# Kernel optimization log

Hardware: AMD Instinct MI355X
Metric: run time of the kernel (lower is better)

The kernel has to match this reference:

```python
import jax, jax.numpy as jnp
import numpy as np
from jax import lax

H, W = 4096, 4096

def setup_inputs() -> dict:
    key = jax.random.key(0)
    k_occ, k_seed = jax.random.split(key)
    occupied = (jax.random.uniform(k_occ, (H, W)) < 0.3).astype(jnp.float32)
    flood = ((jax.random.uniform(k_seed, (H, W)) < 1e-3).astype(jnp.float32)
             * (1.0 - occupied))
    flood_input = jnp.stack([occupied, flood], axis=-1)  # [H, W, 2]
    flood_count = jnp.zeros((H, W), dtype=jnp.float32)
    # Fixed flood kernel, HWIO layout: (3, 3, in=2, out=1)
    kernel = jnp.zeros((3, 3, 2, 1), dtype=jnp.float32)
    kernel = kernel.at[1, 1, 0, 0].set(-5.0)  # occupied center blocks flood
    kernel = kernel.at[1, 2, 1, 0].set(1.0)   # right
    kernel = kernel.at[2, 1, 1, 0].set(1.0)   # down
    kernel = kernel.at[1, 0, 1, 0].set(1.0)   # left
    kernel = kernel.at[0, 1, 1, 0].set(1.0)   # up
    kernel = kernel.at[1, 1, 1, 0].set(1.0)   # center
    bias = jnp.zeros((1,), dtype=jnp.float32)
    return {"flood_input": flood_input, "flood_count": flood_count,
            "kernel": kernel, "bias": bias, "num_steps": 16}

def reference(flood_input, flood_count, kernel, bias, num_steps):
    dn = ("NHWC", "HWIO", "NHWC")

    def flood_step(carry, _):
        x, count = carry                      # x: [H, W, 2], count: [H, W]
        occupied = x[..., 0]
        y = lax.conv_general_dilated(x[None], kernel, (1, 1), "SAME",
                                     dimension_numbers=dn)[0, ..., 0] + bias[0]
        y = jnp.clip(y, 0.0, 1.0)             # flooded frontier
        new_x = jnp.stack([occupied, y], axis=-1)
        return (new_x, count + y), None

    (x_final, count_final), _ = lax.scan(flood_step,
                                         (flood_input, flood_count),
                                         None, length=num_steps)
    # [H, W, 3]: occupied, flood, count
    return jnp.concatenate([x_final, count_final[..., None]], axis=-1)
```

## Files before the change

### kernel.cpp

```cpp
#include <hip/hip_runtime.h>


typedef unsigned long long u64;

#define HH 4096
#define WW 4096
#define WPR 64
#define NSTEPS 16
#define HALO 16
#define IT 32

__global__ __launch_bounds__(256) void pack_kernel(
    const float* __restrict__ flood_input,
    u64* __restrict__ occP, u64* __restrict__ flP)
{
    const int lane = threadIdx.x & 63;
    const int wv   = threadIdx.x >> 6;
    const int r    = blockIdx.x;
#pragma unroll
    for (int b = 0; b < 2; ++b) {
        float vx[8], vy[8];
#pragma unroll
        for (int j = 0; j < 8; ++j) {
            const int w = wv * 16 + b * 8 + j;
            const float2 v = *(const float2*)(flood_input +
                                ((size_t)r * WW + (w << 6) + lane) * 2);
            vx[j] = v.x; vy[j] = v.y;
        }
#pragma unroll
        for (int j = 0; j < 8; ++j) {
            const int w = wv * 16 + b * 8 + j;
            const u64 om = __ballot(vx[j] > 0.5f);
            const u64 fm = __ballot(vy[j] > 0.5f);
            if (lane == 0) {
                occP[(size_t)r * WPR + w] = om;
                flP [(size_t)r * WPR + w] = fm;
            }
        }
    }
}

__global__ __launch_bounds__(256, 8) void flood_kernel(
    const u64* __restrict__ occP, const u64* __restrict__ flP,
    const float* __restrict__ flood_count,
    float* __restrict__ out)
{
    __shared__ u64 plane[4][IT][7];
    __shared__ float out2[4][2 * 128 * 3];

    const int tid  = threadIdx.x;
    const int lane = tid & 63;
    const int wv   = tid >> 6;

    const int tile_r0 = blockIdx.y * IT;
    const int tile_c0 = blockIdx.x * (4 * IT) + wv * IT;
    const int bc0    = blockIdx.x * (4 * IT);

    const int gr  = tile_r0 - HALO + lane;
    const bool rin = (gr >= 0) & (gr < HH);
    const int s   = tile_c0 - HALO;
    const int q0  = ((s + 64) >> 6) - 1;
    const int sh  = s - (q0 << 6);

    const size_t base = (size_t)(rin ? gr : 0) * WPR;
    const int qa = min(max(q0, 0), WPR - 1);
    const int qb = min(max(q0 + 1, 0), WPR - 1);
    u64 o0 = occP[base + qa], o1 = occP[base + qb];
    u64 f0 = flP [base + qa], f1 = flP [base + qb];
    const bool va = rin & (q0 >= 0);
    const bool vb = rin & (q0 + 1 < WPR);
    if (!va) { o0 = ~0ull; f0 = 0ull; }
    if (!vb) { o1 = ~0ull; f1 = 0ull; }
    const u64 occ = (o0 >> sh) | (sh ? (o1 << (64 - sh)) : 0ull);
    u64       f   = (f0 >> sh) | (sh ? (f1 << (64 - sh)) : 0ull);

    const u64 nocc = ~occ;
    u64 c0 = 0, c1 = 0, c2 = 0, c3 = 0, c4 = 0;
#pragma unroll
    for (int it = 0; it < NSTEPS; ++it) {
        u64 up = __shfl_up(f, 1);
        u64 dn = __shfl_down(f, 1);
        if (lane == 0)  up = 0ull;
        if (lane == 63) dn = 0ull;
        f = nocc & (f | (f << 1) | (f >> 1) | up | dn);
        u64 c = f, t;
        t = c0; c0 = t ^ c; c = t & c;
        t = c1; c1 = t ^ c; c = t & c;
        t = c2; c2 = t ^ c; c = t & c;
        t = c3; c3 = t ^ c; c = t & c;
        c4 ^= c;
    }

    if (lane >= HALO && lane < HALO + IT) {
        u64* p = plane[wv][lane - HALO];
        p[0] = occ; p[1] = f;
        p[2] = c0; p[3] = c1; p[4] = c2; p[5] = c3; p[6] = c4;
    }
    __syncthreads();

    const int half = lane >> 5;
    const int l32  = lane & 31;
    for (int t = 0; t < 4; ++t) {
        const int rA   = wv * 8 + 2 * t;
        const int irow = rA + half;
        const int grr  = tile_r0 + irow;
        const int col0 = l32 * 4;

        const float4 fc4 = *(const float4*)(flood_count +
                                (size_t)grr * WW + bc0 + col0);
        const int sw   = col0 >> 5;
        const u64* p   = plane[sw][irow];
        const u64 ow = p[0], fw = p[1];
        const u64 k0 = p[2], k1 = p[3], k2 = p[4], k3 = p[5], k4 = p[6];
        const int bit0 = HALO + (col0 & 31);

        float v[12];
        const float fcv[4] = { fc4.x, fc4.y, fc4.z, fc4.w };
#pragma unroll
        for (int j = 0; j < 4; ++j) {
            const int bit = bit0 + j;
            int cv = (int)((k0 >> bit) & 1ull)
                   + ((int)((k1 >> bit) & 1ull) << 1)
                   + ((int)((k2 >> bit) & 1ull) << 2)
                   + ((int)((k3 >> bit) & 1ull) << 3)
                   + ((int)((k4 >> bit) & 1ull) << 4);
            v[j * 3 + 0] = (float)((ow >> bit) & 1ull);
            v[j * 3 + 1] = (float)((fw >> bit) & 1ull);
            v[j * 3 + 2] = (float)cv + fcv[j];
        }
        float* dst = &out2[wv][half * 384 + l32 * 12];
        *(float4*)(dst + 0) = make_float4(v[0], v[1], v[2],  v[3]);
        *(float4*)(dst + 4) = make_float4(v[4], v[5], v[6],  v[7]);
        *(float4*)(dst + 8) = make_float4(v[8], v[9], v[10], v[11]);

        __syncthreads();

        const float* src = &out2[wv][0];
#pragma unroll
        for (int st = 0; st < 3; ++st) {
            const int L   = st * 256 + lane * 4;
            const int row = (L >= 384) ? 1 : 0;
            const int off = L - row * 384;
            const float4 q = *(const float4*)(src + L);
            *(float4*)(out + ((size_t)(tile_r0 + rA + row) * WW + bc0) * 3 + off) = q;
        }
    }
}

extern "C" void kernel_launch(void* const* d_in, const int* in_sizes, int n_in,
                              void* d_out, int out_size, void* d_ws, size_t ws_size,
                              hipStream_t stream) {
    const float* flood_input = (const float*)d_in[0];
    const float* flood_cnt   = (const float*)d_in[1];
    float* out = (float*)d_out;

    u64* occP = (u64*)d_ws;
    u64* flP  = occP + (size_t)HH * WPR;

    pack_kernel<<<dim3(HH), dim3(256), 0, stream>>>(flood_input, occP, flP);

    dim3 grid(WW / (4 * IT), HH / IT);
    flood_kernel<<<grid, dim3(256), 0, stream>>>(occP, flP, flood_cnt, out);
}
```

Before: 354.3 us.

## Widen per-wave tile to 128 columns using four 64-bit words per lane

Each wavefront now owns a 32-row by 128-column tile. It carries four 64-bit bit-plane words per lane (two interior words plus halo words) instead of one word with a 32-column interior, so the halo overhead per simulated column drops. The block-wide __syncthreads calls are replaced with per-wave LDS waits, since each wave now only reads its own shared-memory region. A prefetch of the next flood_count row is added. In exchange the kernel uses more registers per lane (launch bounds drop to 4 blocks) and more shared memory per block.

```diff
diff --git a/kernel.cpp b/kernel.cpp
--- a/kernel.cpp
+++ b/kernel.cpp
@@ -8,7 +8,8 @@
 #define WPR 64
 #define NSTEPS 16
 #define HALO 16
-#define IT 32
+#define IT_R 32
+#define IT_C 128
 
 __global__ __launch_bounds__(256) void pack_kernel(
     const float* __restrict__ flood_input,
@@ -40,79 +41,94 @@
     }
 }
 
-__global__ __launch_bounds__(256, 8) void flood_kernel(
+__global__ __launch_bounds__(256, 4) void flood_kernel(
     const u64* __restrict__ occP, const u64* __restrict__ flP,
     const float* __restrict__ flood_count,
     float* __restrict__ out)
 {
-    __shared__ u64 plane[4][IT][7];
-    __shared__ float out2[4][2 * 128 * 3];
+    __shared__ u64   plane[4][IT_R][15];
+    __shared__ float out2 [4][2 * IT_C * 3];
 
     const int tid  = threadIdx.x;
     const int lane = tid & 63;
     const int wv   = tid >> 6;
 
-    const int tile_r0 = blockIdx.y * IT;
-    const int tile_c0 = blockIdx.x * (4 * IT) + wv * IT;
-    const int bc0    = blockIdx.x * (4 * IT);
+    const int R0 = blockIdx.y * (4 * IT_R) + wv * IT_R;
+    const int C0 = blockIdx.x * IT_C;
 
-    const int gr  = tile_r0 - HALO + lane;
+    const int gr   = R0 - HALO + lane;
     const bool rin = (gr >= 0) & (gr < HH);
-    const int s   = tile_c0 - HALO;
-    const int q0  = ((s + 64) >> 6) - 1;
-    const int sh  = s - (q0 << 6);
+    const size_t base = (size_t)(rin ? gr : 0) * WPR;
+    const int w0 = (C0 >> 6) - 1;
 
-    const size_t base = (size_t)(rin ? gr : 0) * WPR;
-    const int qa = min(max(q0, 0), WPR - 1);
-    const int qb = min(max(q0 + 1, 0), WPR - 1);
-    u64 o0 = occP[base + qa], o1 = occP[base + qb];
-    u64 f0 = flP [base + qa], f1 = flP [base + qb];
-    const bool va = rin & (q0 >= 0);
-    const bool vb = rin & (q0 + 1 < WPR);
-    if (!va) { o0 = ~0ull; f0 = 0ull; }
-    if (!vb) { o1 = ~0ull; f1 = 0ull; }
-    const u64 occ = (o0 >> sh) | (sh ? (o1 << (64 - sh)) : 0ull);
-    u64       f   = (f0 >> sh) | (sh ? (f1 << (64 - sh)) : 0ull);
+    u64 occ[4], f[4];
+#pragma unroll
+    for (int k = 0; k < 4; ++k) {
+        const int q  = w0 + k;
+        const bool v = rin & (q >= 0) & (q < WPR);
+        const int qc = min(max(q, 0), WPR - 1);
+        const u64 o  = occP[base + qc];
+        const u64 fl = flP [base + qc];
+        occ[k] = v ? o  : ~0ull;
+        f[k]   = v ? fl : 0ull;
+    }
 
-    const u64 nocc = ~occ;
-    u64 c0 = 0, c1 = 0, c2 = 0, c3 = 0, c4 = 0;
+    u64 cA0=0,cA1=0,cA2=0,cA3=0,cA4=0;
+    u64 cB0=0,cB1=0,cB2=0,cB3=0,cB4=0;
 #pragma unroll
     for (int it = 0; it < NSTEPS; ++it) {
-        u64 up = __shfl_up(f, 1);
-        u64 dn = __shfl_down(f, 1);
-        if (lane == 0)  up = 0ull;
-        if (lane == 63) dn = 0ull;
-        f = nocc & (f | (f << 1) | (f >> 1) | up | dn);
-        u64 c = f, t;
-        t = c0; c0 = t ^ c; c = t & c;
-        t = c1; c1 = t ^ c; c = t & c;
-        t = c2; c2 = t ^ c; c = t & c;
-        t = c3; c3 = t ^ c; c = t & c;
-        c4 ^= c;
+        u64 up0=__shfl_up(f[0],1),   up1=__shfl_up(f[1],1),
+            up2=__shfl_up(f[2],1),   up3=__shfl_up(f[3],1);
+        u64 dn0=__shfl_down(f[0],1), dn1=__shfl_down(f[1],1),
+            dn2=__shfl_down(f[2],1), dn3=__shfl_down(f[3],1);
+        if (lane == 0)  { up0=0; up1=0; up2=0; up3=0; }
+        if (lane == 63) { dn0=0; dn1=0; dn2=0; dn3=0; }
+        u64 nf0 = ~occ[0] & (f[0] | (f[0]<<1)               | (f[0]>>1) | (f[1]<<63) | up0 | dn0);
+        u64 nf1 = ~occ[1] & (f[1] | (f[1]<<1) | (f[0]>>63)  | (f[1]>>1) | (f[2]<<63) | up1 | dn1);
+        u64 nf2 = ~occ[2] & (f[2] | (f[2]<<1) | (f[1]>>63)  | (f[2]>>1) | (f[3]<<63) | up2 | dn2);
+        u64 nf3 = ~occ[3] & (f[3] | (f[3]<<1) | (f[2]>>63)  | (f[3]>>1)              | up3 | dn3);
+        u64 c, t;
+        c = nf1;
+        t=cA0; cA0=t^c; c=t&c;  t=cA1; cA1=t^c; c=t&c;
+        t=cA2; cA2=t^c; c=t&c;  t=cA3; cA3=t^c; c=t&c;  cA4^=c;
+        c = nf2;
+        t=cB0; cB0=t^c; c=t&c;  t=cB1; cB1=t^c; c=t&c;
+        t=cB2; cB2=t^c; c=t&c;  t=cB3; cB3=t^c; c=t&c;  cB4^=c;
+        f[0]=nf0; f[1]=nf1; f[2]=nf2; f[3]=nf3;
     }
 
-    if (lane >= HALO && lane < HALO + IT) {
-        u64* p = plane[wv][lane - HALO];
-        p[0] = occ; p[1] = f;
-        p[2] = c0; p[3] = c1; p[4] = c2; p[5] = c3; p[6] = c4;
+    {
+        const int ir = lane - HALO;
+        if (ir >= 0 && ir < IT_R) {
+            u64* p = plane[wv][ir];
+            p[0]=occ[1]; p[1]=occ[2]; p[2]=f[1]; p[3]=f[2];
+            p[4]=cA0; p[5]=cA1; p[6]=cA2; p[7]=cA3; p[8]=cA4;
+            p[9]=cB0; p[10]=cB1; p[11]=cB2; p[12]=cB3; p[13]=cB4;
+        }
     }
-    __syncthreads();
+    asm volatile("s_waitcnt lgkmcnt(0)" ::: "memory");
 
     const int half = lane >> 5;
     const int l32  = lane & 31;
-    for (int t = 0; t < 4; ++t) {
-        const int rA   = wv * 8 + 2 * t;
-        const int irow = rA + half;
-        const int grr  = tile_r0 + irow;
-        const int col0 = l32 * 4;
+    const int col0 = l32 * 4;
+    const int word = col0 >> 6;
+    const int bit0 = col0 & 63;
+    const float* fcbase = flood_count + (size_t)(R0 + half) * WW + C0 + col0;
+    float* outw = out + ((size_t)R0 * WW + C0) * 3;
 
-        const float4 fc4 = *(const float4*)(flood_count +
-                                (size_t)grr * WW + bc0 + col0);
-        const int sw   = col0 >> 5;
-        const u64* p   = plane[sw][irow];
-        const u64 ow = p[0], fw = p[1];
-        const u64 k0 = p[2], k1 = p[3], k2 = p[4], k3 = p[5], k4 = p[6];
-        const int bit0 = HALO + (col0 & 31);
+    float4 fnext = *(const float4*)fcbase;
+    for (int t = 0; t < IT_R / 2; ++t) {
+        const float4 fc4 = fnext;
+        if (t + 1 < IT_R / 2)
+            fnext = *(const float4*)(fcbase + (size_t)(t + 1) * 2 * WW);
+
+        const int irow = t * 2 + half;
+        const u64* p = plane[wv][irow];
+        const u64 ow = p[word];
+        const u64 fw = p[2 + word];
+        const int cb = 4 + word * 5;
+        const u64 k0 = p[cb+0], k1 = p[cb+1], k2 = p[cb+2],
+                  k3 = p[cb+3], k4 = p[cb+4];
 
         float v[12];
         const float fcv[4] = { fc4.x, fc4.y, fc4.z, fc4.w };
@@ -124,25 +140,24 @@
                    + ((int)((k2 >> bit) & 1ull) << 2)
                    + ((int)((k3 >> bit) & 1ull) << 3)
                    + ((int)((k4 >> bit) & 1ull) << 4);
-            v[j * 3 + 0] = (float)((ow >> bit) & 1ull);
-            v[j * 3 + 1] = (float)((fw >> bit) & 1ull);
-            v[j * 3 + 2] = (float)cv + fcv[j];
+            v[j*3+0] = (float)((ow >> bit) & 1ull);
+            v[j*3+1] = (float)((fw >> bit) & 1ull);
+            v[j*3+2] = (float)cv + fcv[j];
         }
         float* dst = &out2[wv][half * 384 + l32 * 12];
         *(float4*)(dst + 0) = make_float4(v[0], v[1], v[2],  v[3]);
         *(float4*)(dst + 4) = make_float4(v[4], v[5], v[6],  v[7]);
         *(float4*)(dst + 8) = make_float4(v[8], v[9], v[10], v[11]);
 
-        __syncthreads();
+        asm volatile("s_waitcnt lgkmcnt(0)" ::: "memory");
 
-        const float* src = &out2[wv][0];
 #pragma unroll
         for (int st = 0; st < 3; ++st) {
             const int L   = st * 256 + lane * 4;
             const int row = (L >= 384) ? 1 : 0;
             const int off = L - row * 384;
-            const float4 q = *(const float4*)(src + L);
-            *(float4*)(out + ((size_t)(tile_r0 + rA + row) * WW + bc0) * 3 + off) = q;
+            const float4 q = *(const float4*)(&out2[wv][L]);
+            *(float4*)(outw + ((size_t)(t * 2 + row) * WW) * 3 + off) = q;
         }
     }
 }
@@ -159,6 +174,6 @@
 
     pack_kernel<<<dim3(HH), dim3(256), 0, stream>>>(flood_input, occP, flP);
 
-    dim3 grid(WW / (4 * IT), HH / IT);
+    dim3 grid(WW / IT_C, HH / (4 * IT_R));
     flood_kernel<<<grid, dim3(256), 0, stream>>>(occP, flP, flood_cnt, out);
 }
```

After: 360.5 us. Within noise of the previous version (+1.8%).

## Make epilogue wave-local and replace block barriers with LDS waitcnt

Applied to the files above, without the earlier changes.

Each wavefront now writes out only its own 32-column sub-tile: 8 rows per pass, with rows padded to 104 floats in shared memory. Because no wave reads another wave's shared data any more, the block-wide __syncthreads calls become s_waitcnt lgkmcnt(0). This is meant to remove barrier stalls between waves. The trade-off is narrower contiguous global stores (384 bytes per row instead of 1536) and reliance on wave-local ordering of LDS accesses.

```diff
diff --git a/kernel.cpp b/kernel.cpp
--- a/kernel.cpp
+++ b/kernel.cpp
@@ -46,7 +46,7 @@
     float* __restrict__ out)
 {
     __shared__ u64 plane[4][IT][7];
-    __shared__ float out2[4][2 * 128 * 3];
+    __shared__ float out2[4][7 * 104 + 96];
 
     const int tid  = threadIdx.x;
     const int lane = tid & 63;
@@ -54,7 +54,6 @@
 
     const int tile_r0 = blockIdx.y * IT;
     const int tile_c0 = blockIdx.x * (4 * IT) + wv * IT;
-    const int bc0    = blockIdx.x * (4 * IT);
 
     const int gr  = tile_r0 - HALO + lane;
     const bool rin = (gr >= 0) & (gr < HH);
@@ -96,23 +95,19 @@
         p[0] = occ; p[1] = f;
         p[2] = c0; p[3] = c1; p[4] = c2; p[5] = c3; p[6] = c4;
     }
-    __syncthreads();
+    asm volatile("s_waitcnt lgkmcnt(0)" ::: "memory");
 
-    const int half = lane >> 5;
-    const int l32  = lane & 31;
+    const int rsub = lane >> 3;
+    const int g    = lane & 7;
+    const int bit0 = HALO + g * 4;
     for (int t = 0; t < 4; ++t) {
-        const int rA   = wv * 8 + 2 * t;
-        const int irow = rA + half;
+        const int irow = t * 8 + rsub;
         const int grr  = tile_r0 + irow;
-        const int col0 = l32 * 4;
-
         const float4 fc4 = *(const float4*)(flood_count +
-                                (size_t)grr * WW + bc0 + col0);
-        const int sw   = col0 >> 5;
-        const u64* p   = plane[sw][irow];
+                                (size_t)grr * WW + tile_c0 + g * 4);
+        const u64* p = plane[wv][irow];
         const u64 ow = p[0], fw = p[1];
         const u64 k0 = p[2], k1 = p[3], k2 = p[4], k3 = p[5], k4 = p[6];
-        const int bit0 = HALO + (col0 & 31);
 
         float v[12];
         const float fcv[4] = { fc4.x, fc4.y, fc4.z, fc4.w };
@@ -124,25 +119,25 @@
                    + ((int)((k2 >> bit) & 1ull) << 2)
                    + ((int)((k3 >> bit) & 1ull) << 3)
                    + ((int)((k4 >> bit) & 1ull) << 4);
-            v[j * 3 + 0] = (float)((ow >> bit) & 1ull);
-            v[j * 3 + 1] = (float)((fw >> bit) & 1ull);
-            v[j * 3 + 2] = (float)cv + fcv[j];
+            v[j*3+0] = (float)((ow >> bit) & 1ull);
+            v[j*3+1] = (float)((fw >> bit) & 1ull);
+            v[j*3+2] = (float)cv + fcv[j];
         }
-        float* dst = &out2[wv][half * 384 + l32 * 12];
+        float* dst = &out2[wv][rsub * 104 + g * 12];
         *(float4*)(dst + 0) = make_float4(v[0], v[1], v[2],  v[3]);
         *(float4*)(dst + 4) = make_float4(v[4], v[5], v[6],  v[7]);
         *(float4*)(dst + 8) = make_float4(v[8], v[9], v[10], v[11]);
 
-        __syncthreads();
+        asm volatile("s_waitcnt lgkmcnt(0)" ::: "memory");
 
-        const float* src = &out2[wv][0];
 #pragma unroll
         for (int st = 0; st < 3; ++st) {
             const int L   = st * 256 + lane * 4;
-            const int row = (L >= 384) ? 1 : 0;
-            const int off = L - row * 384;
-            const float4 q = *(const float4*)(src + L);
-            *(float4*)(out + ((size_t)(tile_r0 + rA + row) * WW + bc0) * 3 + off) = q;
+            const int row = L / 96;
+            const int off = L - row * 96;
+            const float4 q = *(const float4*)(&out2[wv][row * 104 + off]);
+            *(float4*)(out + ((size_t)(tile_r0 + t * 8 + row) * WW
+                              + tile_c0) * 3 + off) = q;
         }
     }
 }
```

Measured after the change: 364.9 us. 3.0% more time.
